# Kernel optimization log

Measured on AMD Instinct MI355X. Metric: run time of the kernel, lower is better.

## Reference

```python
import jax, jax.numpy as jnp
import numpy as np

D_MODEL = 1024
N_HEADS = 16
D_HEAD = D_MODEL // N_HEADS


def setup_inputs() -> dict:
    key = jax.random.key(0)
    k1, k2, k3 = jax.random.split(key, 3)
    B, T = 2, 2048
    x = jax.random.normal(k1, (B, T, D_MODEL), dtype=jnp.float32)
    key_padding_mask = jnp.zeros((B, T), dtype=bool)  # True = padded key
    # nn.Linear weights: [out_features, in_features], bias=False
    W_qkv = jax.random.normal(k2, (3 * D_MODEL, D_MODEL), dtype=jnp.float32) * (D_MODEL ** -0.5)
    W_proj = jax.random.normal(k3, (D_MODEL, D_MODEL), dtype=jnp.float32) * (D_MODEL ** -0.5)
    return {"x": x, "key_padding_mask": key_padding_mask, "W_qkv": W_qkv, "W_proj": W_proj}


def reference(x, key_padding_mask, W_qkv, W_proj):
    B, T, D = x.shape
    H, Dh = N_HEADS, D_HEAD
    scale = Dh ** -0.5
    # qkv: [B,T,3D] -> [3,B,H,T,Dh]
    qkv = (x @ W_qkv.T).reshape(B, T, 3, H, Dh).transpose(2, 0, 3, 1, 4)
    q, k, v = qkv[0], qkv[1], qkv[2]
    # attention scores [B,H,T,T]
    attn = jnp.einsum("bhqd,bhkd->bhqk", q, k) * scale
    attn = jnp.where(key_padding_mask[:, None, None, :], -jnp.inf, attn)
    attn = jax.nn.softmax(attn, axis=-1)  # dropout in eval mode = identity
    out = jnp.einsum("bhqk,bhkd->bhqd", attn, v)
    out = out.transpose(0, 2, 1, 3).reshape(B, T, D)
    return out @ W_proj.T
```

## Files before the change

kernel.cpp:

```cpp
#include <hip/hip_runtime.h>
#include <hip/hip_bf16.h>

typedef unsigned short u16;
typedef unsigned int u32;
typedef __bf16 bf16x8 __attribute__((ext_vector_type(8)));
typedef float f32x4 __attribute__((ext_vector_type(4)));
typedef float f32x16 __attribute__((ext_vector_type(16)));

#define DMODEL 1024
#define NH 16
#define DH 64
#define BB 2
#define TT 2048
#define MM 4096
#define NQKV 3072
#define KVB 128

#define QSCALE 0.18033688011112042f

static __device__ __forceinline__ u16 f2bf(float f) {
  u32 u = __float_as_uint(f);
  u = (u + 0x7FFFu + ((u >> 16) & 1u)) >> 16;
  return (u16)u;
}

static __device__ __forceinline__ u32 pk2bf(float a, float b) {
  u16 ua = __builtin_bit_cast(u16, (__bf16)a);
  u16 ub = __builtin_bit_cast(u16, (__bf16)b);
  return (u32)ua | ((u32)ub << 16);
}

static __device__ __forceinline__ float fexp2(float x) {
#if __has_builtin(__builtin_amdgcn_exp2f)
  return __builtin_amdgcn_exp2f(x);
#else
  float r; asm("v_exp_f32 %0, %1" : "=v"(r) : "v"(x)); return r;
#endif
}

static __device__ __forceinline__ float max3f(float a, float b, float c) {
  return fmaxf(fmaxf(a, b), c);
}

static __device__ __forceinline__ float maxv16(const f32x16& v) {
  float t0 = max3f(v[0], v[1], v[2]);
  float t1 = max3f(v[3], v[4], v[5]);
  float t2 = max3f(v[6], v[7], v[8]);
  float t3 = max3f(v[9], v[10], v[11]);
  float t4 = max3f(v[12], v[13], v[14]);
  return fmaxf(max3f(t0, t1, t2), max3f(t3, t4, v[15]));
}

static __device__ __forceinline__ void gload16(const u16* g, u16* l) {
  __builtin_amdgcn_global_load_lds(
      (const __attribute__((address_space(1))) void*)g,
      (__attribute__((address_space(3))) void*)l, 16, 0, 0);
}

#define N4X  (MM * DMODEL / 4)
#define N4W  (NQKV * DMODEL / 4)
#define N4P  (DMODEL * DMODEL / 4)
__global__ __launch_bounds__(256) void cvt_all(const float* __restrict__ x,
                                               const float* __restrict__ wqkv,
                                               const float* __restrict__ wproj,
                                               u16* __restrict__ dst) {
  int i = blockIdx.x * 256 + threadIdx.x;
  const float* src;
  int j = i;
  if (i < N4X) {
    src = x;
  } else if (i < N4X + N4W) {
    src = wqkv; j = i - N4X;
  } else {
    src = wproj; j = i - (N4X + N4W);
  }
  float4 v = reinterpret_cast<const float4*>(src)[j];
  ushort4 o;
  o.x = f2bf(v.x); o.y = f2bf(v.y); o.z = f2bf(v.z); o.w = f2bf(v.w);
  reinterpret_cast<ushort4*>(dst)[i] = o;
}

static __device__ __forceinline__ void gemm_stage(
    const u16* __restrict__ A, const u16* __restrict__ B, u16* As, u16* Bs,
    int r0, int o0, int r1, int o1, int c0, int c1, int kcol) {
  gload16(A + (size_t)r0 * DMODEL + kcol + o0, As + c0 * 8);
  gload16(A + (size_t)r1 * DMODEL + kcol + o1, As + c1 * 8);
  gload16(B + (size_t)r0 * DMODEL + kcol + o0, Bs + c0 * 8);
  gload16(B + (size_t)r1 * DMODEL + kcol + o1, Bs + c1 * 8);
}

static __device__ __forceinline__ void gemm128_mainloop(
    const u16* __restrict__ Abase, const u16* __restrict__ Bbase,
    u16* As, u16* Bs, f32x4 (&acc)[4][4]) {
  const int tid = threadIdx.x;
  const int lane = tid & 63;
  const int w = tid >> 6;
  const int rowg = lane >> 4, col = lane & 15;
  const int wm = w >> 1, wn = w & 1;
  const int c0 = tid, c1 = tid + 256;
  const int r0 = c0 >> 2, o0 = (c0 & 3) * 8;
  const int r1 = c1 >> 2, o1 = (c1 & 3) * 8;

  gemm_stage(Abase, Bbase, As, Bs, r0, o0, r1, o1, c0, c1, 0);

#define GCOMP(AS, BS)                                                                 \
  {                                                                                   \
    bf16x8 af[4], bfr[4];                                                             \
    _Pragma("unroll") for (int i = 0; i < 4; ++i)                                     \
      af[i] = *reinterpret_cast<const bf16x8*>((AS) + (wm * 64 + i * 16 + col) * 32 + rowg * 8); \
    _Pragma("unroll") for (int j = 0; j < 4; ++j)                                     \
      bfr[j] = *reinterpret_cast<const bf16x8*>((BS) + (wn * 64 + j * 16 + col) * 32 + rowg * 8); \
    _Pragma("unroll") for (int i = 0; i < 4; ++i)                                     \
      _Pragma("unroll") for (int j = 0; j < 4; ++j)                                   \
        acc[i][j] = __builtin_amdgcn_mfma_f32_16x16x32_bf16(af[i], bfr[j], acc[i][j], 0, 0, 0); \
  }

  for (int kt = 0; kt < DMODEL / 32; kt += 2) {
    gemm_stage(Abase, Bbase, As + 4096, Bs + 4096, r0, o0, r1, o1, c0, c1,
               ((kt + 1) & (DMODEL / 32 - 1)) * 32);
    asm volatile("s_waitcnt vmcnt(4)" ::: "memory");
    __builtin_amdgcn_s_barrier();
    __builtin_amdgcn_sched_barrier(0);
    GCOMP(As, Bs);
    __builtin_amdgcn_sched_barrier(0);
    __builtin_amdgcn_s_barrier();
    gemm_stage(Abase, Bbase, As, Bs, r0, o0, r1, o1, c0, c1,
               ((kt + 2) & (DMODEL / 32 - 1)) * 32);
    asm volatile("s_waitcnt vmcnt(4)" ::: "memory");
    __builtin_amdgcn_s_barrier();
    __builtin_amdgcn_sched_barrier(0);
    GCOMP(As + 4096, Bs + 4096);
    __builtin_amdgcn_sched_barrier(0);
    __builtin_amdgcn_s_barrier();
  }
#undef GCOMP
}

__global__ __launch_bounds__(256, 3) void qkv_gemm(
    const u16* __restrict__ xb, const u16* __restrict__ wb,
    u16* __restrict__ qb, u16* __restrict__ kb, u16* __restrict__ vtb) {
  __shared__ u16 As[2 * 128 * 32];
  __shared__ u16 Bs[2 * 128 * 32];
  f32x4 acc[4][4];
#pragma unroll
  for (int i = 0; i < 4; ++i)
#pragma unroll
    for (int j = 0; j < 4; ++j) acc[i][j] = (f32x4){0.f, 0.f, 0.f, 0.f};
  gemm128_mainloop(xb + (size_t)blockIdx.y * 128 * DMODEL,
                   wb + (size_t)blockIdx.x * 128 * DMODEL, As, Bs, acc);
  const int lane = threadIdx.x & 63, w = threadIdx.x >> 6;
  const int rowg = lane >> 4, col = lane & 15, wm = w >> 1, wn = w & 1;
#pragma unroll
  for (int i = 0; i < 4; ++i) {
#pragma unroll
    for (int j = 0; j < 4; ++j) {
#pragma unroll
      for (int r = 0; r < 4; ++r) {
        int m = blockIdx.y * 128 + wm * 64 + i * 16 + rowg * 4 + r;
        int n = blockIdx.x * 128 + wn * 64 + j * 16 + col;
        int b = m >> 11, t = m & (TT - 1);
        int s = n >> 10, h = (n >> 6) & 15, d = n & 63;
        int bh = b * NH + h;
        float v = acc[i][j][r];
        if (s == 0)      qb[((size_t)bh * TT + t) * DH + d] = f2bf(v * QSCALE);
        else if (s == 1) kb[((size_t)bh * TT + t) * DH + d] = f2bf(v);
        else             vtb[((size_t)bh * DH + d) * TT + t] = f2bf(v);
      }
    }
  }
}

__global__ __launch_bounds__(256, 3) void proj_gemm(
    const u16* __restrict__ ab, const u16* __restrict__ wb, float* __restrict__ out) {
  __shared__ u16 As[2 * 128 * 32];
  __shared__ u16 Bs[2 * 128 * 32];
  f32x4 acc[4][4];
#pragma unroll
  for (int i = 0; i < 4; ++i)
#pragma unroll
    for (int j = 0; j < 4; ++j) acc[i][j] = (f32x4){0.f, 0.f, 0.f, 0.f};
  gemm128_mainloop(ab + (size_t)blockIdx.y * 128 * DMODEL,
                   wb + (size_t)blockIdx.x * 128 * DMODEL, As, Bs, acc);
  const int lane = threadIdx.x & 63, w = threadIdx.x >> 6;
  const int rowg = lane >> 4, col = lane & 15, wm = w >> 1, wn = w & 1;
#pragma unroll
  for (int i = 0; i < 4; ++i) {
#pragma unroll
    for (int j = 0; j < 4; ++j) {
#pragma unroll
      for (int r = 0; r < 4; ++r) {
        int m = blockIdx.y * 128 + wm * 64 + i * 16 + rowg * 4 + r;
        int n = blockIdx.x * 128 + wn * 64 + j * 16 + col;
        out[(size_t)m * DMODEL + n] = acc[i][j][r];
      }
    }
  }
}

static __device__ __forceinline__ void attn_stage(
    const u16* __restrict__ kbase, const u16* __restrict__ vbase,
    int kt, u16* KsSel, u16* VsSel, int tid) {
#pragma unroll
  for (int p = 0; p < 4; ++p) {
    int c = p * 256 + tid;
    int row = c >> 3;
    int bI = (c & 7) * 16;
    gload16(kbase + kt * (KVB * DH) + row * DH + ((bI ^ ((row & 7) << 4)) >> 1), KsSel + c * 8);
  }
#pragma unroll
  for (int p = 0; p < 4; ++p) {
    int c = p * 256 + tid;
    int d = c >> 4;
    int bI = (c & 15) * 16;
    gload16(vbase + (size_t)d * TT + kt * KVB + ((bI ^ ((d & 7) << 4)) >> 1), VsSel + c * 8);
  }
}

__global__ __launch_bounds__(256, 2) void attn_kernel(
    const u16* __restrict__ qb, const u16* __restrict__ kb,
    const u16* __restrict__ vtb, const unsigned char* __restrict__ mask,
    u16* __restrict__ ob) {
  __shared__ u16 SM[2][2][KVB * DH];
  __shared__ unsigned char maskb[TT];
  __shared__ u32 mflag;

  const int tid = threadIdx.x;
  const int lane = tid & 63, w = tid >> 6;
  const int col = lane & 31, h = lane >> 5;
  const int qt = blockIdx.x, bh = blockIdx.y;
  const int b = bh >> 4;

  if (tid == 0) mflag = 0;
  __syncthreads();

  {
    const u32* mg = reinterpret_cast<const u32*>(mask + (size_t)b * TT);
    u32 m0 = mg[tid * 2], m1 = mg[tid * 2 + 1];
    *reinterpret_cast<u32*>(maskb + tid * 8) = m0;
    *reinterpret_cast<u32*>(maskb + tid * 8 + 4) = m1;
    if (m0 | m1) atomicOr(&mflag, 1u << (tid >> 4));
  }

  const int qrow0 = qt * 128 + w * 32;
  const u16* qptr = qb + ((size_t)bh * TT + qrow0) * DH;
  bf16x8 aq[4];
#pragma unroll
  for (int dstep = 0; dstep < 4; ++dstep)
    aq[dstep] = *reinterpret_cast<const bf16x8*>(qptr + col * DH + dstep * 16 + h * 8);

  f32x16 acc[2];
#pragma unroll
  for (int df = 0; df < 2; ++df)
#pragma unroll
    for (int r = 0; r < 16; ++r) acc[df][r] = 0.f;
  float m_run = -1e30f, l_run = 0.f;

  const u16* kbase = kb + (size_t)bh * TT * DH;
  const u16* vbase = vtb + (size_t)bh * DH * TT;

  attn_stage(kbase, vbase, 0, SM[0][0], SM[0][1], tid);
  __syncthreads();
  const u32 fm = mflag;

#define ATILE(T, KS, VS)                                                              \
  do {                                                                                \
    const int t_ = (T);                                                               \
    f32x16 sc[4];                                                                     \
    _Pragma("unroll") for (int kf = 0; kf < 4; ++kf)                                  \
      _Pragma("unroll") for (int r = 0; r < 16; ++r) sc[kf][r] = 0.f;                 \
    _Pragma("unroll") for (int dstep = 0; dstep < 4; ++dstep) {                       \
      bf16x8 ak[4];                                                                   \
      _Pragma("unroll") for (int kf = 0; kf < 4; ++kf) {                              \
        int row = kf * 32 + col;                                                      \
        ak[kf] = *reinterpret_cast<const bf16x8*>(                                    \
            (KS) + row * DH + (((dstep * 32 + h * 16) ^ ((row & 7) << 4)) >> 1));     \
      }                                                                               \
      _Pragma("unroll") for (int kf = 0; kf < 4; ++kf)                                \
        sc[kf] = __builtin_amdgcn_mfma_f32_32x32x16_bf16(ak[kf], aq[dstep], sc[kf], 0, 0, 0); \
    }                                                                                 \
    if (fm & (1u << t_)) {                                                            \
      _Pragma("unroll") for (int kf = 0; kf < 4; ++kf)                                \
        _Pragma("unroll") for (int r = 0; r < 16; ++r) {                              \
          int key = kf * 32 + (r & 3) + 8 * (r >> 2) + 4 * h;                         \
          sc[kf][r] += maskb[t_ * KVB + key] ? -1e30f : 0.f;                          \
        }                                                                             \
    }                                                                                 \
    u32 P2[4][8];                                                                     \
    {                                                                                 \
      float mk0 = maxv16(sc[0]), mk1 = maxv16(sc[1]);                                 \
      float mk2 = maxv16(sc[2]), mk3 = maxv16(sc[3]);                                 \
      float mx = fmaxf(fmaxf(mk0, mk1), fmaxf(mk2, mk3));                             \
      mx = fmaxf(mx, __shfl_xor(mx, 32, 64));                                         \
      if (__any(mx > m_run + 8.0f)) {                                                 \
        float mn = fmaxf(m_run, mx);                                                  \
        float corr = fexp2(m_run - mn);                                               \
        m_run = mn;                                                                   \
        l_run *= corr;                                                                \
        _Pragma("unroll") for (int df = 0; df < 2; ++df)                              \
          _Pragma("unroll") for (int r = 0; r < 16; ++r) acc[df][r] *= corr;          \
      }                                                                               \
      const float mc = m_run;                                                         \
      float rs = 0.f;                                                                 \
      _Pragma("unroll") for (int kf = 0; kf < 4; ++kf) {                              \
        _Pragma("unroll") for (int i = 0; i < 8; ++i) {                               \
          float p0 = fexp2(sc[kf][2 * i] - mc);                                       \
          float p1 = fexp2(sc[kf][2 * i + 1] - mc);                                   \
          rs += p0 + p1;                                                              \
          P2[kf][i] = pk2bf(p0, p1);                                                  \
        }                                                                             \
      }                                                                               \
      rs += __shfl_xor(rs, 32, 64);                                                   \
      l_run += rs;                                                                    \
    }                                                                                 \
    __builtin_amdgcn_s_setprio(1);                                                    \
    _Pragma("unroll") for (int ksl = 0; ksl < 8; ++ksl) {                             \
      const int kf = ksl >> 1;                                                        \
      const int i0 = (ksl & 1) * 4;                                                   \
      u32 w0 = P2[kf][i0],     w2 = P2[kf][i0 + 2];                                   \
      u32 w1 = P2[kf][i0 + 1], w3 = P2[kf][i0 + 3];                                   \
      asm("v_permlane32_swap_b32 %0, %1" : "+v"(w0), "+v"(w2));                       \
      asm("v_permlane32_swap_b32 %0, %1" : "+v"(w1), "+v"(w3));                       \
      u32 bpw[4] = {w0, w1, w2, w3};                                                  \
      bf16x8 bp = __builtin_bit_cast(bf16x8, *reinterpret_cast<uint4*>(bpw));         \
      _Pragma("unroll") for (int df = 0; df < 2; ++df) {                              \
        int row = df * 32 + col;                                                      \
        bf16x8 av = *reinterpret_cast<const bf16x8*>(                                 \
            (VS) + row * KVB + (((ksl * 32 + h * 16) ^ ((row & 7) << 4)) >> 1));      \
        acc[df] = __builtin_amdgcn_mfma_f32_32x32x16_bf16(av, bp, acc[df], 0, 0, 0);  \
      }                                                                               \
    }                                                                                 \
    __builtin_amdgcn_s_setprio(0);                                                    \
  } while (0)

  for (int t = 0; t < TT / KVB; t += 2) {
    attn_stage(kbase, vbase, t + 1, SM[1][0], SM[1][1], tid);
    asm volatile("s_waitcnt vmcnt(8)" ::: "memory");
    __builtin_amdgcn_s_barrier();
    __builtin_amdgcn_sched_barrier(0);
    ATILE(t, SM[0][0], SM[0][1]);
    __builtin_amdgcn_sched_barrier(0);
    __builtin_amdgcn_s_barrier();
    attn_stage(kbase, vbase, (t + 2) & (TT / KVB - 1), SM[0][0], SM[0][1], tid);
    asm volatile("s_waitcnt vmcnt(8)" ::: "memory");
    __builtin_amdgcn_s_barrier();
    __builtin_amdgcn_sched_barrier(0);
    ATILE(t + 1, SM[1][0], SM[1][1]);
    __builtin_amdgcn_sched_barrier(0);
    __builtin_amdgcn_s_barrier();
  }
#undef ATILE

  asm volatile("s_waitcnt vmcnt(0)" ::: "memory");
  __builtin_amdgcn_s_barrier();

  u16* Ol = &SM[0][0][0];
  {
    float inv = 1.f / l_run;
    const int q = w * 32 + col;
    const int swzq = (q ^ (q >> 3)) & 7;
#pragma unroll
    for (int df = 0; df < 2; ++df) {
#pragma unroll
      for (int a = 0; a < 4; ++a) {
        uint2 pk;
        pk.x = pk2bf(acc[df][4 * a] * inv, acc[df][4 * a + 1] * inv);
        pk.y = pk2bf(acc[df][4 * a + 2] * inv, acc[df][4 * a + 3] * inv);
        int d2 = df * 64 + a * 16 + h * 8;
        int byte = q * 128 + (d2 ^ (swzq << 4));
        *reinterpret_cast<uint2*>(reinterpret_cast<char*>(Ol) + byte) = pk;
      }
    }
  }
  __syncthreads();
  {
    const int hh = bh & 15;
#pragma unroll
    for (int p = 0; p < 4; ++p) {
      int idx = p * 256 + tid;
      int q = idx >> 3, ch = idx & 7;
      int swzq = (q ^ (q >> 3)) & 7;
      uint4 v = *reinterpret_cast<const uint4*>(
          reinterpret_cast<const char*>(Ol) + q * 128 + ((ch * 16) ^ (swzq << 4)));
      size_t row = (size_t)(b * TT + qt * 128 + q);
      *reinterpret_cast<uint4*>(ob + row * DMODEL + hh * DH + ch * 8) = v;
    }
  }
}

extern "C" void kernel_launch(void* const* d_in, const int* in_sizes, int n_in,
                              void* d_out, int out_size, void* d_ws, size_t ws_size,
                              hipStream_t stream) {
  const float* x = (const float*)d_in[0];
  const unsigned char* mask = (const unsigned char*)d_in[1];
  const float* wqkv = (const float*)d_in[2];
  const float* wproj = (const float*)d_in[3];
  float* out = (float*)d_out;

  u16* xb     = (u16*)d_ws;
  u16* wqkvb  = xb    + (size_t)MM * DMODEL;
  u16* wprojb = wqkvb + (size_t)NQKV * DMODEL;
  u16* qb     = wprojb + (size_t)DMODEL * DMODEL;
  u16* kb     = qb + (size_t)MM * DMODEL;
  u16* vtb    = kb + (size_t)MM * DMODEL;
  u16* ob     = vtb + (size_t)MM * DMODEL;

  cvt_all<<<(N4X + N4W + N4P) / 256, 256, 0, stream>>>(x, wqkv, wproj, xb);
  qkv_gemm<<<dim3(NQKV / 128, MM / 128), 256, 0, stream>>>(xb, wqkvb, qb, kb, vtb);
  attn_kernel<<<dim3(TT / 128, BB * NH), 256, 0, stream>>>(qb, kb, vtb, mask, ob);
  proj_gemm<<<dim3(DMODEL / 128, MM / 128), 256, 0, stream>>>(ob, wprojb, out);
}
```

Before: 128.4 us.

## Rewrite QKV GEMM with 256x256 tiles, 8 waves, swizzled LDS and phased pipeline

Replaces the 128x128 QKV GEMM with a 256x256-tile, 512-thread kernel using a 64-wide K step and XOR-swizzled LDS addressing to avoid bank conflicts. Loads are split into four half-tile phases interleaved with MFMA work, with s_setprio raised around the MFMA bursts. The larger tile raises arithmetic intensity, but the grid shrinks to 192 blocks, which may underfill the 256 CUs on MI355X. The projection GEMM is inlined unchanged.

Result: slower. 152.3 us (+18.7%).

```diff
diff --git a/kernel.cpp b/kernel.cpp
--- a/kernel.cpp
+++ b/kernel.cpp
@@ -80,6 +80,124 @@
   reinterpret_cast<ushort4*>(dst)[i] = o;
 }
 
+static __device__ __forceinline__ void stageA_mh(const u16* __restrict__ Ab, u16* ld,
+                                                 int mh, int tt, int tid) {
+#pragma unroll
+  for (int p = 0; p < 2; ++p) {
+    int rl = p * 64 + (tid >> 3);
+    int r  = (rl & 63) + ((rl >> 6) << 7) + mh * 64;
+    int sb = (tid & 7) * 16;
+    gload16(Ab + (size_t)r * DMODEL + tt * 64 + ((sb ^ ((r & 7) << 4)) >> 1),
+            ld + r * 64 + (tid & 7) * 8);
+  }
+}
+static __device__ __forceinline__ void stageB_nh(const u16* __restrict__ Bb, u16* ld,
+                                                 int nh, int tt, int tid) {
+#pragma unroll
+  for (int p = 0; p < 2; ++p) {
+    int rl = p * 64 + (tid >> 3);
+    int r  = (rl & 31) + ((rl >> 5) << 6) + nh * 32;
+    int sb = (tid & 7) * 16;
+    gload16(Bb + (size_t)r * DMODEL + tt * 64 + ((sb ^ ((r & 7) << 4)) >> 1),
+            ld + r * 64 + (tid & 7) * 8);
+  }
+}
+
+__global__ __launch_bounds__(512, 2) void qkv_gemm(
+    const u16* __restrict__ xb, const u16* __restrict__ wb,
+    u16* __restrict__ qb, u16* __restrict__ kb, u16* __restrict__ vtb) {
+  __shared__ u16 As[2 * 256 * 64];
+  __shared__ u16 Bs[2 * 256 * 64];
+  const int tid = threadIdx.x;
+  const int lane = tid & 63;
+  const int wid = tid >> 6;
+  const int wm = wid >> 2, wn = wid & 3;
+  const u16* Ab = xb + (size_t)blockIdx.y * 256 * DMODEL;
+  const u16* Bb = wb + (size_t)blockIdx.x * 256 * DMODEL;
+
+  f32x4 acc[8][4];
+#pragma unroll
+  for (int i = 0; i < 8; ++i)
+#pragma unroll
+    for (int j = 0; j < 4; ++j) acc[i][j] = (f32x4){0.f, 0.f, 0.f, 0.f};
+
+  stageA_mh(Ab, As, 0, 0, tid);
+  stageB_nh(Bb, Bs, 0, 0, tid);
+  stageA_mh(Ab, As, 1, 0, tid);
+  stageB_nh(Bb, Bs, 1, 0, tid);
+  stageA_mh(Ab, As + 16384, 0, 1, tid);
+  stageB_nh(Bb, Bs + 16384, 0, 1, tid);
+  asm volatile("s_waitcnt vmcnt(4)" ::: "memory");
+  __builtin_amdgcn_s_barrier();
+
+#define QPHASE(MH, NH, STAGE_STMT, VMCNT_STMT)                                        \
+  {                                                                                   \
+    bf16x8 af[4][2], bfq[2][2];                                                       \
+    _Pragma("unroll") for (int i = 0; i < 4; ++i) {                                   \
+      int row = wm * 128 + (MH) * 64 + i * 16 + (lane & 15);                          \
+      _Pragma("unroll") for (int ks = 0; ks < 2; ++ks)                                \
+        af[i][ks] = *reinterpret_cast<const bf16x8*>(                                 \
+            asd + row * 64 + (((ks * 64 + (lane >> 4) * 16) ^ ((row & 7) << 4)) >> 1)); \
+    }                                                                                 \
+    _Pragma("unroll") for (int j = 0; j < 2; ++j) {                                   \
+      int row = wn * 64 + (NH) * 32 + j * 16 + (lane & 15);                           \
+      _Pragma("unroll") for (int ks = 0; ks < 2; ++ks)                                \
+        bfq[j][ks] = *reinterpret_cast<const bf16x8*>(                                \
+            bsd + row * 64 + (((ks * 64 + (lane >> 4) * 16) ^ ((row & 7) << 4)) >> 1)); \
+    }                                                                                 \
+    STAGE_STMT;                                                                       \
+    __builtin_amdgcn_s_barrier();                                                     \
+    asm volatile("s_waitcnt lgkmcnt(0)" ::: "memory");                                \
+    __builtin_amdgcn_sched_barrier(0);                                                \
+    __builtin_amdgcn_s_setprio(1);                                                    \
+    _Pragma("unroll") for (int ks = 0; ks < 2; ++ks)                                  \
+      _Pragma("unroll") for (int i = 0; i < 4; ++i)                                   \
+        _Pragma("unroll") for (int j = 0; j < 2; ++j)                                 \
+          acc[(MH) * 4 + i][(NH) * 2 + j] = __builtin_amdgcn_mfma_f32_16x16x32_bf16(  \
+              af[i][ks], bfq[j][ks], acc[(MH) * 4 + i][(NH) * 2 + j], 0, 0, 0);       \
+    __builtin_amdgcn_s_setprio(0);                                                    \
+    __builtin_amdgcn_sched_barrier(0);                                                \
+    VMCNT_STMT;                                                                       \
+    __builtin_amdgcn_s_barrier();                                                     \
+  }
+
+  for (int t = 0; t < DMODEL / 64; ++t) {
+    const int d = t & 1;
+    const u16* asd = As + d * 16384;
+    const u16* bsd = Bs + d * 16384;
+    u16* asn = As + (d ^ 1) * 16384;
+    u16* bsn = Bs + (d ^ 1) * 16384;
+    u16* asc = As + d * 16384;
+    u16* bsc = Bs + d * 16384;
+    QPHASE(0, 0, stageA_mh(Ab, asn, 1, (t + 1) & 15, tid), );
+    QPHASE(0, 1, stageB_nh(Bb, bsn, 1, (t + 1) & 15, tid), );
+    QPHASE(1, 0, stageA_mh(Ab, asc, 0, (t + 2) & 15, tid), );
+    QPHASE(1, 1, stageB_nh(Bb, bsc, 0, (t + 2) & 15, tid),
+           asm volatile("s_waitcnt vmcnt(4)" ::: "memory"));
+  }
+#undef QPHASE
+
+  const int rowg = lane >> 4, col = lane & 15;
+#pragma unroll
+  for (int mi = 0; mi < 8; ++mi) {
+#pragma unroll
+    for (int nj = 0; nj < 4; ++nj) {
+#pragma unroll
+      for (int r = 0; r < 4; ++r) {
+        int m = blockIdx.y * 256 + wm * 128 + mi * 16 + rowg * 4 + r;
+        int n = blockIdx.x * 256 + wn * 64 + nj * 16 + col;
+        int b = m >> 11, t = m & (TT - 1);
+        int s = n >> 10, h = (n >> 6) & 15, d = n & 63;
+        int bh = b * NH + h;
+        float v = acc[mi][nj][r];
+        if (s == 0)      qb[((size_t)bh * TT + t) * DH + d] = f2bf(v * QSCALE);
+        else if (s == 1) kb[((size_t)bh * TT + t) * DH + d] = f2bf(v);
+        else             vtb[((size_t)bh * DH + d) * TT + t] = f2bf(v);
+      }
+    }
+  }
+}
+
 static __device__ __forceinline__ void gemm_stage(
     const u16* __restrict__ A, const u16* __restrict__ B, u16* As, u16* Bs,
     int r0, int o0, int r1, int o1, int c0, int c1, int kcol) {
@@ -89,9 +207,10 @@
   gload16(B + (size_t)r1 * DMODEL + kcol + o1, Bs + c1 * 8);
 }
 
-static __device__ __forceinline__ void gemm128_mainloop(
-    const u16* __restrict__ Abase, const u16* __restrict__ Bbase,
-    u16* As, u16* Bs, f32x4 (&acc)[4][4]) {
+__global__ __launch_bounds__(256, 3) void proj_gemm(
+    const u16* __restrict__ ab, const u16* __restrict__ wb, float* __restrict__ out) {
+  __shared__ u16 As[2 * 128 * 32];
+  __shared__ u16 Bs[2 * 128 * 32];
   const int tid = threadIdx.x;
   const int lane = tid & 63;
   const int w = tid >> 6;
@@ -100,6 +219,14 @@
   const int c0 = tid, c1 = tid + 256;
   const int r0 = c0 >> 2, o0 = (c0 & 3) * 8;
   const int r1 = c1 >> 2, o1 = (c1 & 3) * 8;
+  const u16* Abase = ab + (size_t)blockIdx.y * 128 * DMODEL;
+  const u16* Bbase = wb + (size_t)blockIdx.x * 128 * DMODEL;
+
+  f32x4 acc[4][4];
+#pragma unroll
+  for (int i = 0; i < 4; ++i)
+#pragma unroll
+    for (int j = 0; j < 4; ++j) acc[i][j] = (f32x4){0.f, 0.f, 0.f, 0.f};
 
   gemm_stage(Abase, Bbase, As, Bs, r0, o0, r1, o1, c0, c1, 0);
 
@@ -134,55 +261,7 @@
     __builtin_amdgcn_s_barrier();
   }
 #undef GCOMP
-}
-
-__global__ __launch_bounds__(256, 3) void qkv_gemm(
-    const u16* __restrict__ xb, const u16* __restrict__ wb,
-    u16* __restrict__ qb, u16* __restrict__ kb, u16* __restrict__ vtb) {
-  __shared__ u16 As[2 * 128 * 32];
-  __shared__ u16 Bs[2 * 128 * 32];
-  f32x4 acc[4][4];
-#pragma unroll
-  for (int i = 0; i < 4; ++i)
-#pragma unroll
-    for (int j = 0; j < 4; ++j) acc[i][j] = (f32x4){0.f, 0.f, 0.f, 0.f};
-  gemm128_mainloop(xb + (size_t)blockIdx.y * 128 * DMODEL,
-                   wb + (size_t)blockIdx.x * 128 * DMODEL, As, Bs, acc);
-  const int lane = threadIdx.x & 63, w = threadIdx.x >> 6;
-  const int rowg = lane >> 4, col = lane & 15, wm = w >> 1, wn = w & 1;
-#pragma unroll
-  for (int i = 0; i < 4; ++i) {
-#pragma unroll
-    for (int j = 0; j < 4; ++j) {
-#pragma unroll
-      for (int r = 0; r < 4; ++r) {
-        int m = blockIdx.y * 128 + wm * 64 + i * 16 + rowg * 4 + r;
-        int n = blockIdx.x * 128 + wn * 64 + j * 16 + col;
-        int b = m >> 11, t = m & (TT - 1);
-        int s = n >> 10, h = (n >> 6) & 15, d = n & 63;
-        int bh = b * NH + h;
-        float v = acc[i][j][r];
-        if (s == 0)      qb[((size_t)bh * TT + t) * DH + d] = f2bf(v * QSCALE);
-        else if (s == 1) kb[((size_t)bh * TT + t) * DH + d] = f2bf(v);
-        else             vtb[((size_t)bh * DH + d) * TT + t] = f2bf(v);
-      }
-    }
-  }
-}
-
-__global__ __launch_bounds__(256, 3) void proj_gemm(
-    const u16* __restrict__ ab, const u16* __restrict__ wb, float* __restrict__ out) {
-  __shared__ u16 As[2 * 128 * 32];
-  __shared__ u16 Bs[2 * 128 * 32];
-  f32x4 acc[4][4];
-#pragma unroll
-  for (int i = 0; i < 4; ++i)
-#pragma unroll
-    for (int j = 0; j < 4; ++j) acc[i][j] = (f32x4){0.f, 0.f, 0.f, 0.f};
-  gemm128_mainloop(ab + (size_t)blockIdx.y * 128 * DMODEL,
-                   wb + (size_t)blockIdx.x * 128 * DMODEL, As, Bs, acc);
-  const int lane = threadIdx.x & 63, w = threadIdx.x >> 6;
-  const int rowg = lane >> 4, col = lane & 15, wm = w >> 1, wn = w & 1;
+
 #pragma unroll
   for (int i = 0; i < 4; ++i) {
 #pragma unroll
@@ -405,7 +484,7 @@
   u16* ob     = vtb + (size_t)MM * DMODEL;
 
   cvt_all<<<(N4X + N4W + N4P) / 256, 256, 0, stream>>>(x, wqkv, wproj, xb);
-  qkv_gemm<<<dim3(NQKV / 128, MM / 128), 256, 0, stream>>>(xb, wqkvb, qb, kb, vtb);
+  qkv_gemm<<<dim3(NQKV / 256, MM / 256), 512, 0, stream>>>(xb, wqkvb, qb, kb, vtb);
   attn_kernel<<<dim3(TT / 128, BB * NH), 256, 0, stream>>>(qb, kb, vtb, mask, ob);
   proj_gemm<<<dim3(DMODEL / 128, MM / 128), 256, 0, stream>>>(ob, wprojb, out);
 }
```
